# Performance work log

Hardware: AMD Instinct MI355X
Metric: run time of the kernel (lower is better)

## Reference

```python
import jax, jax.numpy as jnp
import numpy as np

H = 8        # num attention heads
DH = 160     # head dim (hidden_size // H)
HS = 1280    # hidden_size
CAD = 768    # cross_attention_dim
R = 4        # LoRA rank
LORA_SCALE = 1.0  # `scale` forward arg (default 1.0)


def setup_inputs() -> dict:
    key = jax.random.key(0)
    ks = jax.random.split(key, 16)
    rn = lambda k, s, std=0.02: (jax.random.normal(k, s) * std).astype(jnp.float32)
    return {
        "hidden_states": jax.random.normal(ks[0], (8, 4096, HS), jnp.float32),
        "encoder_hidden_states": jax.random.normal(ks[1], (8, 77, CAD), jnp.float32),
        # base attention projections (nn.Linear weight layout: [out, in])
        "Wq": rn(ks[2], (HS, HS)),
        "Wk": rn(ks[3], (HS, CAD)),
        "Wv": rn(ks[4], (HS, CAD)),
        "Wo": rn(ks[5], (HS, HS)),
        "bo": jnp.zeros((HS,), jnp.float32),
        # LoRA down/up pairs (down std ~ 1/rank; up nonzero so grads flow)
        "q_down": rn(ks[6], (R, HS), 0.25), "q_up": rn(ks[7], (HS, R)),
        "k_down": rn(ks[8], (R, CAD), 0.25), "k_up": rn(ks[9], (HS, R)),
        "v_down": rn(ks[10], (R, CAD), 0.25), "v_up": rn(ks[11], (HS, R)),
        "o_down": rn(ks[12], (R, HS), 0.25), "o_up": rn(ks[13], (HS, R)),
    }


def reference(hidden_states, encoder_hidden_states, Wq, Wk, Wv, Wo, bo,
              q_down, q_up, k_down, k_up, v_down, v_up, o_down, o_up):
    B, S, _ = hidden_states.shape
    T = encoder_hidden_states.shape[1]
    lora = lambda x, d, u: (x @ d.T) @ u.T  # LoRALinearLayer: up(down(x))

    q = hidden_states @ Wq.T + LORA_SCALE * lora(hidden_states, q_down, q_up)
    k = encoder_hidden_states @ Wk.T + LORA_SCALE * lora(encoder_hidden_states, k_down, k_up)
    v = encoder_hidden_states @ Wv.T + LORA_SCALE * lora(encoder_hidden_states, v_down, v_up)

    q = q.reshape(B, S, H, DH)
    k = k.reshape(B, T, H, DH)
    v = v.reshape(B, T, H, DH)

    # attn.get_attention_scores: scaled QK^T, softmax (no mask)
    inv_sqrt_d = jnp.asarray(1.0 / np.sqrt(DH), q.dtype)
    scores = jnp.einsum('bshd,bthd->bhst', q, k) * inv_sqrt_d
    probs = jax.nn.softmax(scores, axis=-1)
    o = jnp.einsum('bhst,bthd->bshd', probs, v).reshape(B, S, H * DH)

    # to_out[0] (Linear with bias) + LoRA on the same input; to_out[1] dropout = identity (eval)
    return o @ Wo.T + bo + LORA_SCALE * lora(o, o_down, o_up)
```

## Files before the change

kernel.cpp:

```cpp
#include <hip/hip_runtime.h>
#include <hip/hip_bf16.h>
#include <stdint.h>

typedef short bf16x8 __attribute__((ext_vector_type(8)));
typedef float f32x4 __attribute__((ext_vector_type(4)));

#define DEVI static __device__ __forceinline__

DEVI ushort f2bf(float f) {
  union { float f; uint32_t u; } v; v.f = f;
  uint32_t u = v.u;
  return (ushort)((u + 0x7fffu + ((u >> 16) & 1u)) >> 16);
}

DEVI void gload16(const void* g, void* l) {
  __builtin_amdgcn_global_load_lds((const __attribute__((address_space(1))) void*)g,
                                   (__attribute__((address_space(3))) void*)l,
                                   16, 0, 0);
}

#define SB() __builtin_amdgcn_sched_barrier(0)
#define BAR() __builtin_amdgcn_s_barrier()
#define MFMA(a, b, c) __builtin_amdgcn_mfma_f32_16x16x32_bf16((a), (b), (c), 0, 0, 0)
#define KEY4(r) ((((r) & 3)) ^ (((r) >> 2) & 3))

__global__ __launch_bounds__(256) void cvt_hs(const float* __restrict__ in,
                                              ushort* __restrict__ out) {
  const long step = 2048L * 256;
  for (long idx = (long)blockIdx.x * 256 + threadIdx.x; idx < 5242880; idx += step) {
    const float4* p = (const float4*)(in + idx * 8);
    float4 a = p[0], b = p[1];
    union { ushort us[8]; uint4 v; } r;
    r.us[0] = f2bf(a.x); r.us[1] = f2bf(a.y); r.us[2] = f2bf(a.z); r.us[3] = f2bf(a.w);
    r.us[4] = f2bf(b.x); r.us[5] = f2bf(b.y); r.us[6] = f2bf(b.z); r.us[7] = f2bf(b.w);
    *(uint4*)(out + idx * 8) = r.v;
  }
}

__global__ __launch_bounds__(256) void fold_t(
    const float* __restrict__ W, const float* __restrict__ up,
    const float* __restrict__ down, ushort* __restrict__ outT, float scale)
{
  __shared__ ushort tile[64][66];
  const int o0 = blockIdx.x * 64, i0 = blockIdx.y * 64;
  const int lo = threadIdx.x >> 6;
  const int li = threadIdx.x & 63;
#pragma unroll
  for (int r = 0; r < 16; ++r) {
    int o = o0 + r * 4 + lo;
    int i = i0 + li;
    float v = W[(long)o * 1280 + i];
#pragma unroll
    for (int q = 0; q < 4; ++q) v += up[o * 4 + q] * down[q * 1280 + i];
    tile[li][r * 4 + lo] = f2bf(v * scale);
  }
  __syncthreads();
#pragma unroll
  for (int r = 0; r < 16; ++r) {
    int i = i0 + r * 4 + lo;
    outT[(long)i * 1280 + o0 + li] = tile[r * 4 + lo][li];
  }
}

__global__ __launch_bounds__(256) void smalls(
    const float* __restrict__ ehs, ushort* __restrict__ ehs_bf,
    const float* __restrict__ Wk, const float* __restrict__ k_up, const float* __restrict__ k_down,
    const float* __restrict__ Wv, const float* __restrict__ v_up, const float* __restrict__ v_down,
    ushort* __restrict__ Wkv,
    const float* __restrict__ Wo, const float* __restrict__ o_up, const float* __restrict__ o_down,
    ushort* __restrict__ Wo_bf, ushort* __restrict__ Nt)
{
  const int b = blockIdx.x;
  const int tid = threadIdx.x;
  if (b < 231) {
    int idx = b * 256 + tid;
    if (idx < 59136) {
      const float4* p = (const float4*)(ehs + (long)idx * 8);
      float4 a = p[0], c = p[1];
      union { ushort us[8]; uint4 v; } r;
      r.us[0] = f2bf(a.x); r.us[1] = f2bf(a.y); r.us[2] = f2bf(a.z); r.us[3] = f2bf(a.w);
      r.us[4] = f2bf(c.x); r.us[5] = f2bf(c.y); r.us[6] = f2bf(c.z); r.us[7] = f2bf(c.w);
      *(uint4*)(ehs_bf + (long)idx * 8) = r.v;
    }
  } else if (b < 4071) {
    int idx = (b - 231) * 256 + tid;
    int o = idx / 768, i = idx - o * 768;
    float v = Wk[idx];
#pragma unroll
    for (int q = 0; q < 4; ++q) v += k_up[o * 4 + q] * k_down[q * 768 + i];
    Wkv[idx] = f2bf(v);
  } else if (b < 7911) {
    int idx = (b - 4071) * 256 + tid;
    int o = idx / 768, i = idx - o * 768;
    float v = Wv[idx];
#pragma unroll
    for (int q = 0; q < 4; ++q) v += v_up[o * 4 + q] * v_down[q * 768 + i];
    Wkv[983040 + idx] = f2bf(v);
  } else if (b < 14311) {
    int idx = (b - 7911) * 256 + tid;
    int o = idx / 1280, i = idx - o * 1280;
    float v = Wo[idx];
#pragma unroll
    for (int q = 0; q < 4; ++q) v += o_up[o * 4 + q] * o_down[q * 1280 + i];
    Wo_bf[idx] = f2bf(v);
  } else {
    int idx = (b - 14311) * 256 + tid;
    int bb = idx / (1280 * 24);
    int rem = idx % (1280 * 24);
    int j = rem / 24, q = rem % 24;
    int h = q / 3, t = 77 + q % 3;
    Nt[(long)bb * 1280 * 640 + (long)j * 640 + h * 80 + t] = 0;
  }
}


__global__ __launch_bounds__(256) void gemm_bt(
    const ushort* __restrict__ A, long sA0, long sA1, int lda, int validM,
    const ushort* __restrict__ B, long sB0, long sB1, int ldb, int validN,
    float* __restrict__ C32, ushort* __restrict__ C16, long sC0, long sC1, int ldc,
    const float* __restrict__ bias, int K)
{
  __shared__ ushort As[128 * 32];
  __shared__ ushort Bs[128 * 32];

  const int z = blockIdx.z;
  const ushort* Ab = A + (long)(z >> 3) * sA0 + (long)(z & 7) * sA1;
  const ushort* Bb = B + (long)(z >> 3) * sB0 + (long)(z & 7) * sB1;
  const int m0 = blockIdx.x * 128;
  const int n0 = blockIdx.y * 128;
  const int tid = threadIdx.x;
  const int lane = tid & 63;
  const int wid = tid >> 6;

  const int c0 = tid;
  const int arow0 = min(m0 + (c0 >> 2), validM - 1);
  const int arow1 = min(m0 + (c0 >> 2) + 64, validM - 1);
  const int brow0 = min(n0 + (c0 >> 2), validN - 1);
  const int brow1 = min(n0 + (c0 >> 2) + 64, validN - 1);
  const int seg = (c0 & 3) * 8;

  const int wr = (wid >> 1) * 64;
  const int wc = (wid & 1) * 64;
  const int frow = lane & 15;
  const int fk = (lane >> 4) * 8;

  f32x4 acc[4][4] = {};

  for (int kt = 0; kt < K; kt += 32) {
    gload16(Ab + (long)arow0 * lda + kt + seg, As + c0 * 8);
    gload16(Ab + (long)arow1 * lda + kt + seg, As + (c0 + 256) * 8);
    gload16(Bb + (long)brow0 * ldb + kt + seg, Bs + c0 * 8);
    gload16(Bb + (long)brow1 * ldb + kt + seg, Bs + (c0 + 256) * 8);
    __syncthreads();

    bf16x8 af[4], bfr[4];
#pragma unroll
    for (int m = 0; m < 4; ++m)
      af[m] = *(const bf16x8*)(As + (wr + m * 16 + frow) * 32 + fk);
#pragma unroll
    for (int n = 0; n < 4; ++n)
      bfr[n] = *(const bf16x8*)(Bs + (wc + n * 16 + frow) * 32 + fk);
#pragma unroll
    for (int m = 0; m < 4; ++m)
#pragma unroll
      for (int n = 0; n < 4; ++n)
        acc[m][n] = MFMA(af[m], bfr[n], acc[m][n]);
    __syncthreads();
  }

  const long cb = (long)(z >> 3) * sC0 + (long)(z & 7) * sC1;
  const int crow = m0 + wr + (lane >> 4) * 4;
  const int ccol = n0 + wc + (lane & 15);
#pragma unroll
  for (int m = 0; m < 4; ++m)
#pragma unroll
    for (int n = 0; n < 4; ++n)
#pragma unroll
      for (int j = 0; j < 4; ++j) {
        int r = crow + m * 16 + j;
        int c = ccol + n * 16;
        if (r < validM && c < validN) {
          float v = acc[m][n][j];
          if (bias) v += bias[c];
          if (C32) C32[cb + (long)r * ldc + c] = v;
          else     C16[cb + (long)r * ldc + c] = f2bf(v);
        }
      }
}

__global__ __launch_bounds__(256, 3) void score_softmax(
    const ushort* __restrict__ hsb, const ushort* __restrict__ Mt,
    ushort* __restrict__ probs)
{
  __shared__ ushort lds[22528];

  const int z = blockIdx.z;
  const int s0 = blockIdx.x * 128;
  const int h0 = blockIdx.y * 2;
  const int tid = threadIdx.x;
  const int lane = tid & 63;
  const int wid = tid >> 6;
  const int wM = wid >> 1;
  const int wN = wid & 1;
  const int l15 = lane & 15;
  const int l4 = lane >> 4;
  const int sl = tid & 3;

  const ushort* Ag = hsb + ((long)z * 4096 + s0) * 1280;
  long asrc[2]; int adst[2];
#pragma unroll
  for (int j = 0; j < 2; ++j) {
    int r = j * 64 + (tid >> 2);
    asrc[j] = (long)r * 1280 + ((sl ^ KEY4(r)) * 8);
    adst[j] = (j * 256 + tid) * 8;
  }
  const ushort* Bg = Mt + (long)z * (640L * 1280);
  long bsrc[3]; int bdst[3];
#pragma unroll
  for (int j = 0; j < 3; ++j) {
    int rb = j * 64 + (tid >> 2);
    int c = h0 * 96 + rb;
    int hh = c / 96, tt = min(c - hh * 96, 76);
    bsrc[j] = (long)(hh * 77 + tt) * 1280 + ((sl ^ KEY4(rb)) * 8);
    bdst[j] = 4096 + (j * 256 + tid) * 8;
  }

  int aoff[4], boff[6];
#pragma unroll
  for (int m = 0; m < 4; ++m) {
    int r = wM * 64 + m * 16 + l15;
    aoff[m] = r * 32 + ((l4 ^ KEY4(r)) * 8);
  }
#pragma unroll
  for (int n = 0; n < 6; ++n) {
    int r = wN * 96 + n * 16 + l15;
    boff[n] = 4096 + r * 32 + ((l4 ^ KEY4(r)) * 8);
  }

  f32x4 acc[4][6] = {};

#define SS_STAGE(bb, kt) { \
    _Pragma("unroll") for (int j = 0; j < 2; ++j) gload16(Ag + asrc[j] + (kt), &lds[(bb) + adst[j]]); \
    _Pragma("unroll") for (int j = 0; j < 3; ++j) gload16(Bg + bsrc[j] + (kt), &lds[(bb) + bdst[j]]); }

  SS_STAGE(0, 0)

  for (int t = 0; t < 40; ++t) {
    const int base = (t & 1) * 10240;
    if (t + 1 < 40) {
      SS_STAGE(10240 - base, (t + 1) * 32)
      asm volatile("s_waitcnt vmcnt(5)" ::: "memory");
    } else {
      asm volatile("s_waitcnt vmcnt(0)" ::: "memory");
    }
    SB(); BAR(); SB();
    bf16x8 av[4], bv[6];
#pragma unroll
    for (int m = 0; m < 4; ++m) av[m] = *(const bf16x8*)(&lds[base + aoff[m]]);
#pragma unroll
    for (int n = 0; n < 6; ++n) bv[n] = *(const bf16x8*)(&lds[base + boff[n]]);
    __builtin_amdgcn_s_setprio(1);
#pragma unroll
    for (int m = 0; m < 4; ++m)
#pragma unroll
      for (int n = 0; n < 6; ++n)
        acc[m][n] = MFMA(av[m], bv[n], acc[m][n]);
    __builtin_amdgcn_s_setprio(0);
    SB(); BAR();
  }
#undef SS_STAGE

#pragma unroll
  for (int m = 0; m < 4; ++m)
#pragma unroll
    for (int j = 0; j < 4; ++j) {
      float mx = -1e30f;
#pragma unroll
      for (int n = 0; n < 6; ++n)
        if (n * 16 + l15 < 77) mx = fmaxf(mx, acc[m][n][j]);
#pragma unroll
      for (int o = 8; o; o >>= 1) mx = fmaxf(mx, __shfl_xor(mx, o));
      float sum = 0.f;
#pragma unroll
      for (int n = 0; n < 6; ++n) {
        float e = (n * 16 + l15 < 77) ? __expf(acc[m][n][j] - mx) : 0.f;
        acc[m][n][j] = e;
        sum += e;
      }
#pragma unroll
      for (int o = 8; o; o >>= 1) sum += __shfl_xor(sum, o);
      float inv = 1.f / sum;
#pragma unroll
      for (int n = 0; n < 6; ++n) acc[m][n][j] *= inv;
    }

  __syncthreads();
  ushort* pw = lds + wid * 5632;
#pragma unroll
  for (int m = 0; m < 4; ++m)
#pragma unroll
    for (int n = 0; n < 5; ++n)
#pragma unroll
      for (int j = 0; j < 4; ++j)
        pw[(m * 16 + l4 * 4 + j) * 88 + n * 16 + l15] = f2bf(acc[m][n][j]);

  const uint* pw32 = (const uint*)pw;
  uint* probs32 = (uint*)probs;
  const int head = h0 + wN;
  const long sbase = (long)z * 4096 + s0 + wM * 64;
#pragma unroll 4
  for (int k = 0; k < 40; ++k) {
    int f2 = k * 64 + lane;
    int r = f2 / 40;
    int tp = f2 - r * 40;
    probs32[(sbase + r) * 320 + head * 40 + tp] = pw32[r * 44 + tp];
  }
}

__global__ __launch_bounds__(256, 4) void gemm_out(
    const ushort* __restrict__ P, const ushort* __restrict__ Nt,
    float* __restrict__ C, const float* __restrict__ bias)
{
  __shared__ ushort lds[16384];

  const int z = blockIdx.z;
  const ushort* Ab = P + (long)z * (4096L * 640) + (long)blockIdx.x * 128 * 640;
  const ushort* Bb = Nt + (long)z * (1280L * 640) + (long)blockIdx.y * 128 * 640;
  const int tid = threadIdx.x;
  const int lane = tid & 63;
  const int wid = tid >> 6;
  const int wM = wid >> 1;
  const int wN = wid & 1;
  const int l15 = lane & 15;
  const int l4 = lane >> 4;
  const int sl = tid & 3;

  long asrc[2]; int adst[2], bdst[2];
#pragma unroll
  for (int j = 0; j < 2; ++j) {
    int r = j * 64 + (tid >> 2);
    asrc[j] = (long)r * 640 + ((sl ^ KEY4(r)) * 8);
    adst[j] = (j * 256 + tid) * 8;
    bdst[j] = 4096 + (j * 256 + tid) * 8;
  }

  int aoff[4], boff[4];
#pragma unroll
  for (int m = 0; m < 4; ++m) {
    int r = wM * 64 + m * 16 + l15;
    aoff[m] = r * 32 + ((l4 ^ KEY4(r)) * 8);
  }
#pragma unroll
  for (int n = 0; n < 4; ++n) {
    int r = wN * 64 + n * 16 + l15;
    boff[n] = 4096 + r * 32 + ((l4 ^ KEY4(r)) * 8);
  }

  f32x4 acc[4][4] = {};

#define OG_STAGE(bb, kt) { \
    _Pragma("unroll") for (int j = 0; j < 2; ++j) gload16(Ab + asrc[j] + (kt), &lds[(bb) + adst[j]]); \
    _Pragma("unroll") for (int j = 0; j < 2; ++j) gload16(Bb + asrc[j] + (kt), &lds[(bb) + bdst[j]]); }

  OG_STAGE(0, 0)

  for (int t = 0; t < 20; ++t) {
    const int base = (t & 1) * 8192;
    if (t + 1 < 20) {
      OG_STAGE(8192 - base, (t + 1) * 32)
      asm volatile("s_waitcnt vmcnt(4)" ::: "memory");
    } else {
      asm volatile("s_waitcnt vmcnt(0)" ::: "memory");
    }
    SB(); BAR(); SB();
    bf16x8 av[4], bv[4];
#pragma unroll
    for (int m = 0; m < 4; ++m) av[m] = *(const bf16x8*)(&lds[base + aoff[m]]);
#pragma unroll
    for (int n = 0; n < 4; ++n) bv[n] = *(const bf16x8*)(&lds[base + boff[n]]);
    __builtin_amdgcn_s_setprio(1);
#pragma unroll
    for (int m = 0; m < 4; ++m)
#pragma unroll
      for (int n = 0; n < 4; ++n)
        acc[m][n] = MFMA(av[m], bv[n], acc[m][n]);
    __builtin_amdgcn_s_setprio(0);
    SB(); BAR();
  }
#undef OG_STAGE

  __syncthreads();
  float* pw = (float*)lds + wid * 1088;
  const int ccol = blockIdx.y * 128 + wN * 64;
  const float4 bv4 = *(const float4*)(bias + ccol + l15 * 4);
  const long crow0 = (long)z * 4096 + blockIdx.x * 128 + wM * 64;
#pragma unroll
  for (int m = 0; m < 4; ++m) {
#pragma unroll
    for (int n = 0; n < 4; ++n)
#pragma unroll
      for (int j = 0; j < 4; ++j)
        pw[(l4 * 4 + j) * 68 + n * 16 + l15] = acc[m][n][j];
    asm volatile("s_waitcnt lgkmcnt(0)" ::: "memory"); SB();
#pragma unroll
    for (int pass = 0; pass < 4; ++pass) {
      int r = pass * 4 + l4;
      float4 v = *(const float4*)(pw + r * 68 + l15 * 4);
      v.x += bv4.x; v.y += bv4.y; v.z += bv4.z; v.w += bv4.w;
      *(float4*)(C + (crow0 + m * 16 + r) * 1280 + ccol + l15 * 4) = v;
    }
    asm volatile("s_waitcnt lgkmcnt(0)" ::: "memory"); SB();
  }
}

extern "C" void kernel_launch(void* const* d_in, const int* in_sizes, int n_in,
                              void* d_out, int out_size, void* d_ws, size_t ws_size,
                              hipStream_t stream) {
  (void)in_sizes; (void)n_in; (void)out_size; (void)ws_size;
  const float* hs     = (const float*)d_in[0];
  const float* ehs    = (const float*)d_in[1];
  const float* Wq     = (const float*)d_in[2];
  const float* Wk     = (const float*)d_in[3];
  const float* Wv     = (const float*)d_in[4];
  const float* Wo     = (const float*)d_in[5];
  const float* bo     = (const float*)d_in[6];
  const float* q_down = (const float*)d_in[7];
  const float* q_up   = (const float*)d_in[8];
  const float* k_down = (const float*)d_in[9];
  const float* k_up   = (const float*)d_in[10];
  const float* v_down = (const float*)d_in[11];
  const float* v_up   = (const float*)d_in[12];
  const float* o_down = (const float*)d_in[13];
  const float* o_up   = (const float*)d_in[14];

  char* w = (char*)d_ws;
  size_t off = 0;
  auto alloc = [&](size_t b) { char* p = w + off; off = (off + b + 255) & ~(size_t)255; return p; };
  ushort* hs_bf  = (ushort*)alloc(32768L * 1280 * 2);
  ushort* ehs_bf = (ushort*)alloc(616L * 768 * 2);
  ushort* WqT    = (ushort*)alloc(1280L * 1280 * 2);
  ushort* Wkv    = (ushort*)alloc(2560L * 768 * 2);
  ushort* Wo_bf  = (ushort*)alloc(1280L * 1280 * 2);
  ushort* kv_bf  = (ushort*)alloc(616L * 2560 * 2);
  ushort* Mt     = (ushort*)alloc(8L * 640 * 1280 * 2);
  ushort* Nt     = (ushort*)alloc(8L * 1280 * 640 * 2);
  ushort* probs  = (ushort*)alloc(8L * 4096 * 640 * 2);
  float*  outp   = (float*)d_out;
  const float invs = 0.07905694150420949f;

  cvt_hs<<<2048, 256, 0, stream>>>(hs, hs_bf);
  fold_t<<<dim3(20, 20), 256, 0, stream>>>(Wq, q_up, q_down, WqT, invs);
  smalls<<<15271, 256, 0, stream>>>(ehs, ehs_bf,
      Wk, k_up, k_down, Wv, v_up, v_down, Wkv,
      Wo, o_up, o_down, Wo_bf, Nt);
  gemm_bt<<<dim3(5, 20, 1), 256, 0, stream>>>(ehs_bf, 0, 0, 768, 616,
      Wkv, 0, 0, 768, 2560, nullptr, kv_bf, 0, 0, 2560, nullptr, 768);
  gemm_bt<<<dim3(1, 10, 64), 256, 0, stream>>>(kv_bf, 77L * 2560, 160, 2560, 77,
      WqT, 0, 160, 1280, 1280, nullptr, Mt, 640L * 1280, 77L * 1280, 1280, nullptr, 160);
  gemm_bt<<<dim3(10, 1, 64), 256, 0, stream>>>(Wo_bf, 0, 160, 1280, 1280,
      kv_bf + 1280, 77L * 2560, 160, 2560, 77, nullptr, Nt, 1280L * 640, 80, 640, nullptr, 160);
  score_softmax<<<dim3(32, 4, 8), 256, 0, stream>>>(hs_bf, Mt, probs);
  gemm_out<<<dim3(32, 10, 8), 256, 0, stream>>>(probs, Nt, outp, bo);
}
```

Baseline: 283.7 us.

## Merge prep kernels and Mt/Nt GEMMs, switch LDS swizzle to paired-row layout

Folds the hs conversion, Wq fold/transpose and small-weight prep into one prep launch, and runs the two per-head Mt and Nt GEMMs in a single launch. This removes several kernel launches and their tail gaps. It also replaces the KEY4 XOR swizzle in score_softmax and gemm_out with a two-rows-per-64-element paired layout meant to reduce LDS bank conflicts. gemm_out gets a larger LDS array, which may lower occupancy.

```diff
diff --git a/kernel.cpp b/kernel.cpp
--- a/kernel.cpp
+++ b/kernel.cpp
@@ -22,47 +22,22 @@
 #define SB() __builtin_amdgcn_sched_barrier(0)
 #define BAR() __builtin_amdgcn_s_barrier()
 #define MFMA(a, b, c) __builtin_amdgcn_mfma_f32_16x16x32_bf16((a), (b), (c), 0, 0, 0)
-#define KEY4(r) ((((r) & 3)) ^ (((r) >> 2) & 3))
-
-__global__ __launch_bounds__(256) void cvt_hs(const float* __restrict__ in,
-                                              ushort* __restrict__ out) {
-  const long step = 2048L * 256;
-  for (long idx = (long)blockIdx.x * 256 + threadIdx.x; idx < 5242880; idx += step) {
-    const float4* p = (const float4*)(in + idx * 8);
-    float4 a = p[0], b = p[1];
-    union { ushort us[8]; uint4 v; } r;
-    r.us[0] = f2bf(a.x); r.us[1] = f2bf(a.y); r.us[2] = f2bf(a.z); r.us[3] = f2bf(a.w);
-    r.us[4] = f2bf(b.x); r.us[5] = f2bf(b.y); r.us[6] = f2bf(b.z); r.us[7] = f2bf(b.w);
-    *(uint4*)(out + idx * 8) = r.v;
-  }
-}
-
-__global__ __launch_bounds__(256) void fold_t(
-    const float* __restrict__ W, const float* __restrict__ up,
-    const float* __restrict__ down, ushort* __restrict__ outT, float scale)
-{
-  __shared__ ushort tile[64][66];
-  const int o0 = blockIdx.x * 64, i0 = blockIdx.y * 64;
-  const int lo = threadIdx.x >> 6;
-  const int li = threadIdx.x & 63;
-#pragma unroll
-  for (int r = 0; r < 16; ++r) {
-    int o = o0 + r * 4 + lo;
-    int i = i0 + li;
-    float v = W[(long)o * 1280 + i];
-#pragma unroll
-    for (int q = 0; q < 4; ++q) v += up[o * 4 + q] * down[q * 1280 + i];
-    tile[li][r * 4 + lo] = f2bf(v * scale);
-  }
-  __syncthreads();
-#pragma unroll
-  for (int r = 0; r < 16; ++r) {
-    int i = i0 + r * 4 + lo;
-    outT[(long)i * 1280 + o0 + li] = tile[r * 4 + lo][li];
-  }
-}
-
-__global__ __launch_bounds__(256) void smalls(
+
+DEVI int pair_src_row(int c, int* k8) {
+  int pair = c >> 3;
+  int s = (c & 7) ^ (pair & 7);
+  *k8 = s >> 1;
+  return pair * 2 + (s & 1);
+}
+DEVI int pair_frag_off(int r, int k8) {
+  int p = (k8 * 2 + (r & 1)) ^ ((r >> 1) & 7);
+  return (r >> 1) * 64 + p * 8;
+}
+
+__global__ __launch_bounds__(256) void prep(
+    const float* __restrict__ hs, ushort* __restrict__ hs_bf,
+    const float* __restrict__ Wq, const float* __restrict__ q_up, const float* __restrict__ q_down,
+    ushort* __restrict__ WqT, float scale,
     const float* __restrict__ ehs, ushort* __restrict__ ehs_bf,
     const float* __restrict__ Wk, const float* __restrict__ k_up, const float* __restrict__ k_down,
     const float* __restrict__ Wv, const float* __restrict__ v_up, const float* __restrict__ v_down,
@@ -70,64 +45,94 @@
     const float* __restrict__ Wo, const float* __restrict__ o_up, const float* __restrict__ o_down,
     ushort* __restrict__ Wo_bf, ushort* __restrict__ Nt)
 {
+  __shared__ ushort tile[64][66];
   const int b = blockIdx.x;
   const int tid = threadIdx.x;
-  if (b < 231) {
-    int idx = b * 256 + tid;
-    if (idx < 59136) {
-      const float4* p = (const float4*)(ehs + (long)idx * 8);
+  if (b < 2048) {
+    const long step = 2048L * 256;
+    for (long idx = (long)b * 256 + tid; idx < 5242880; idx += step) {
+      const float4* p = (const float4*)(hs + idx * 8);
       float4 a = p[0], c = p[1];
       union { ushort us[8]; uint4 v; } r;
       r.us[0] = f2bf(a.x); r.us[1] = f2bf(a.y); r.us[2] = f2bf(a.z); r.us[3] = f2bf(a.w);
       r.us[4] = f2bf(c.x); r.us[5] = f2bf(c.y); r.us[6] = f2bf(c.z); r.us[7] = f2bf(c.w);
-      *(uint4*)(ehs_bf + (long)idx * 8) = r.v;
-    }
-  } else if (b < 4071) {
-    int idx = (b - 231) * 256 + tid;
-    int o = idx / 768, i = idx - o * 768;
-    float v = Wk[idx];
-#pragma unroll
-    for (int q = 0; q < 4; ++q) v += k_up[o * 4 + q] * k_down[q * 768 + i];
-    Wkv[idx] = f2bf(v);
-  } else if (b < 7911) {
-    int idx = (b - 4071) * 256 + tid;
-    int o = idx / 768, i = idx - o * 768;
-    float v = Wv[idx];
-#pragma unroll
-    for (int q = 0; q < 4; ++q) v += v_up[o * 4 + q] * v_down[q * 768 + i];
-    Wkv[983040 + idx] = f2bf(v);
-  } else if (b < 14311) {
-    int idx = (b - 7911) * 256 + tid;
-    int o = idx / 1280, i = idx - o * 1280;
-    float v = Wo[idx];
-#pragma unroll
-    for (int q = 0; q < 4; ++q) v += o_up[o * 4 + q] * o_down[q * 1280 + i];
-    Wo_bf[idx] = f2bf(v);
+      *(uint4*)(hs_bf + idx * 8) = r.v;
+    }
+  } else if (b < 2448) {
+    const int fb = b - 2048;
+    const int o0 = (fb / 20) * 64, i0 = (fb % 20) * 64;
+    const int lo = tid >> 6;
+    const int li = tid & 63;
+#pragma unroll
+    for (int r = 0; r < 16; ++r) {
+      int o = o0 + r * 4 + lo;
+      int i = i0 + li;
+      float v = Wq[(long)o * 1280 + i];
+#pragma unroll
+      for (int q = 0; q < 4; ++q) v += q_up[o * 4 + q] * q_down[q * 1280 + i];
+      tile[li][r * 4 + lo] = f2bf(v * scale);
+    }
+    __syncthreads();
+#pragma unroll
+    for (int r = 0; r < 16; ++r) {
+      int i = i0 + r * 4 + lo;
+      WqT[(long)i * 1280 + o0 + li] = tile[r * 4 + lo][li];
+    }
   } else {
-    int idx = (b - 14311) * 256 + tid;
-    int bb = idx / (1280 * 24);
-    int rem = idx % (1280 * 24);
-    int j = rem / 24, q = rem % 24;
-    int h = q / 3, t = 77 + q % 3;
-    Nt[(long)bb * 1280 * 640 + (long)j * 640 + h * 80 + t] = 0;
-  }
-}
-
-
-__global__ __launch_bounds__(256) void gemm_bt(
+    const int sb = b - 2448;
+    if (sb < 231) {
+      int idx = sb * 256 + tid;
+      if (idx < 59136) {
+        const float4* p = (const float4*)(ehs + (long)idx * 8);
+        float4 a = p[0], c = p[1];
+        union { ushort us[8]; uint4 v; } r;
+        r.us[0] = f2bf(a.x); r.us[1] = f2bf(a.y); r.us[2] = f2bf(a.z); r.us[3] = f2bf(a.w);
+        r.us[4] = f2bf(c.x); r.us[5] = f2bf(c.y); r.us[6] = f2bf(c.z); r.us[7] = f2bf(c.w);
+        *(uint4*)(ehs_bf + (long)idx * 8) = r.v;
+      }
+    } else if (sb < 4071) {
+      int idx = (sb - 231) * 256 + tid;
+      int o = idx / 768, i = idx - o * 768;
+      float v = Wk[idx];
+#pragma unroll
+      for (int q = 0; q < 4; ++q) v += k_up[o * 4 + q] * k_down[q * 768 + i];
+      Wkv[idx] = f2bf(v);
+    } else if (sb < 7911) {
+      int idx = (sb - 4071) * 256 + tid;
+      int o = idx / 768, i = idx - o * 768;
+      float v = Wv[idx];
+#pragma unroll
+      for (int q = 0; q < 4; ++q) v += v_up[o * 4 + q] * v_down[q * 768 + i];
+      Wkv[983040 + idx] = f2bf(v);
+    } else if (sb < 14311) {
+      int idx = (sb - 7911) * 256 + tid;
+      int o = idx / 1280, i = idx - o * 1280;
+      float v = Wo[idx];
+#pragma unroll
+      for (int q = 0; q < 4; ++q) v += o_up[o * 4 + q] * o_down[q * 1280 + i];
+      Wo_bf[idx] = f2bf(v);
+    } else {
+      int idx = (sb - 14311) * 256 + tid;
+      int bb = idx / (1280 * 24);
+      int rem = idx % (1280 * 24);
+      int j = rem / 24, q = rem % 24;
+      int h = q / 3, t = 77 + q % 3;
+      Nt[(long)bb * 1280 * 640 + (long)j * 640 + h * 80 + t] = 0;
+    }
+  }
+}
+
+
+DEVI void gemm_bt_body(int bx, int by, int z,
     const ushort* __restrict__ A, long sA0, long sA1, int lda, int validM,
     const ushort* __restrict__ B, long sB0, long sB1, int ldb, int validN,
     float* __restrict__ C32, ushort* __restrict__ C16, long sC0, long sC1, int ldc,
-    const float* __restrict__ bias, int K)
-{
-  __shared__ ushort As[128 * 32];
-  __shared__ ushort Bs[128 * 32];
-
-  const int z = blockIdx.z;
+    const float* __restrict__ bias, int K, ushort* As, ushort* Bs)
+{
   const ushort* Ab = A + (long)(z >> 3) * sA0 + (long)(z & 7) * sA1;
   const ushort* Bb = B + (long)(z >> 3) * sB0 + (long)(z & 7) * sB1;
-  const int m0 = blockIdx.x * 128;
-  const int n0 = blockIdx.y * 128;
+  const int m0 = bx * 128;
+  const int n0 = by * 128;
   const int tid = threadIdx.x;
   const int lane = tid & 63;
   const int wid = tid >> 6;
@@ -188,6 +193,37 @@
       }
 }
 
+__global__ __launch_bounds__(256) void gemm_bt(
+    const ushort* A, long sA0, long sA1, int lda, int validM,
+    const ushort* B, long sB0, long sB1, int ldb, int validN,
+    float* C32, ushort* C16, long sC0, long sC1, int ldc,
+    const float* bias, int K)
+{
+  __shared__ ushort As[128 * 32];
+  __shared__ ushort Bs[128 * 32];
+  gemm_bt_body(blockIdx.x, blockIdx.y, blockIdx.z,
+               A, sA0, sA1, lda, validM, B, sB0, sB1, ldb, validN,
+               C32, C16, sC0, sC1, ldc, bias, K, As, Bs);
+}
+
+__global__ __launch_bounds__(256) void gemm_mtnt(
+    const ushort* __restrict__ kv_bf, const ushort* __restrict__ WqT,
+    const ushort* __restrict__ Wo_bf, ushort* __restrict__ Mt, ushort* __restrict__ Nt)
+{
+  __shared__ ushort As[128 * 32];
+  __shared__ ushort Bs[128 * 32];
+  const int x = blockIdx.x, z = blockIdx.z;
+  if (x < 10) {
+    gemm_bt_body(x, 0, z, Wo_bf, 0, 160, 1280, 1280,
+                 kv_bf + 1280, 77L * 2560, 160, 2560, 77,
+                 nullptr, Nt, 1280L * 640, 80, 640, nullptr, 160, As, Bs);
+  } else {
+    gemm_bt_body(0, x - 10, z, kv_bf, 77L * 2560, 160, 2560, 77,
+                 WqT, 0, 160, 1280, 1280,
+                 nullptr, Mt, 640L * 1280, 77L * 1280, 1280, nullptr, 160, As, Bs);
+  }
+}
+
 __global__ __launch_bounds__(256, 3) void score_softmax(
     const ushort* __restrict__ hsb, const ushort* __restrict__ Mt,
     ushort* __restrict__ probs)
@@ -204,38 +240,35 @@
   const int wN = wid & 1;
   const int l15 = lane & 15;
   const int l4 = lane >> 4;
-  const int sl = tid & 3;
 
   const ushort* Ag = hsb + ((long)z * 4096 + s0) * 1280;
   long asrc[2]; int adst[2];
 #pragma unroll
   for (int j = 0; j < 2; ++j) {
-    int r = j * 64 + (tid >> 2);
-    asrc[j] = (long)r * 1280 + ((sl ^ KEY4(r)) * 8);
-    adst[j] = (j * 256 + tid) * 8;
+    int c = j * 256 + tid, k8;
+    int r = pair_src_row(c, &k8);
+    asrc[j] = (long)r * 1280 + k8 * 8;
+    adst[j] = c * 8;
   }
   const ushort* Bg = Mt + (long)z * (640L * 1280);
   long bsrc[3]; int bdst[3];
 #pragma unroll
   for (int j = 0; j < 3; ++j) {
-    int rb = j * 64 + (tid >> 2);
-    int c = h0 * 96 + rb;
-    int hh = c / 96, tt = min(c - hh * 96, 76);
-    bsrc[j] = (long)(hh * 77 + tt) * 1280 + ((sl ^ KEY4(rb)) * 8);
-    bdst[j] = 4096 + (j * 256 + tid) * 8;
+    int c = j * 256 + tid, k8;
+    int rb = pair_src_row(c, &k8);
+    int hh = h0 + (rb >= 96);
+    int tt = min(rb - 96 * (rb >= 96), 76);
+    bsrc[j] = (long)(hh * 77 + tt) * 1280 + k8 * 8;
+    bdst[j] = 4096 + c * 8;
   }
 
   int aoff[4], boff[6];
 #pragma unroll
-  for (int m = 0; m < 4; ++m) {
-    int r = wM * 64 + m * 16 + l15;
-    aoff[m] = r * 32 + ((l4 ^ KEY4(r)) * 8);
-  }
-#pragma unroll
-  for (int n = 0; n < 6; ++n) {
-    int r = wN * 96 + n * 16 + l15;
-    boff[n] = 4096 + r * 32 + ((l4 ^ KEY4(r)) * 8);
-  }
+  for (int m = 0; m < 4; ++m)
+    aoff[m] = pair_frag_off(wM * 64 + m * 16 + l15, l4);
+#pragma unroll
+  for (int n = 0; n < 6; ++n)
+    boff[n] = 4096 + pair_frag_off(wN * 96 + n * 16 + l15, l4);
 
   f32x4 acc[4][6] = {};
 
@@ -321,7 +354,7 @@
     const ushort* __restrict__ P, const ushort* __restrict__ Nt,
     float* __restrict__ C, const float* __restrict__ bias)
 {
-  __shared__ ushort lds[16384];
+  __shared__ ushort lds[17408];
 
   const int z = blockIdx.z;
   const ushort* Ab = P + (long)z * (4096L * 640) + (long)blockIdx.x * 128 * 640;
@@ -333,28 +366,24 @@
   const int wN = wid & 1;
   const int l15 = lane & 15;
   const int l4 = lane >> 4;
-  const int sl = tid & 3;
 
   long asrc[2]; int adst[2], bdst[2];
 #pragma unroll
   for (int j = 0; j < 2; ++j) {
-    int r = j * 64 + (tid >> 2);
-    asrc[j] = (long)r * 640 + ((sl ^ KEY4(r)) * 8);
-    adst[j] = (j * 256 + tid) * 8;
-    bdst[j] = 4096 + (j * 256 + tid) * 8;
+    int c = j * 256 + tid, k8;
+    int r = pair_src_row(c, &k8);
+    asrc[j] = (long)r * 640 + k8 * 8;
+    adst[j] = c * 8;
+    bdst[j] = 4096 + c * 8;
   }
 
   int aoff[4], boff[4];
 #pragma unroll
-  for (int m = 0; m < 4; ++m) {
-    int r = wM * 64 + m * 16 + l15;
-    aoff[m] = r * 32 + ((l4 ^ KEY4(r)) * 8);
-  }
-#pragma unroll
-  for (int n = 0; n < 4; ++n) {
-    int r = wN * 64 + n * 16 + l15;
-    boff[n] = 4096 + r * 32 + ((l4 ^ KEY4(r)) * 8);
-  }
+  for (int m = 0; m < 4; ++m)
+    aoff[m] = pair_frag_off(wM * 64 + m * 16 + l15, l4);
+#pragma unroll
+  for (int n = 0; n < 4; ++n)
+    boff[n] = 4096 + pair_frag_off(wN * 64 + n * 16 + l15, l4);
 
   f32x4 acc[4][4] = {};
 
@@ -448,17 +477,12 @@
   float*  outp   = (float*)d_out;
   const float invs = 0.07905694150420949f;
 
-  cvt_hs<<<2048, 256, 0, stream>>>(hs, hs_bf);
-  fold_t<<<dim3(20, 20), 256, 0, stream>>>(Wq, q_up, q_down, WqT, invs);
-  smalls<<<15271, 256, 0, stream>>>(ehs, ehs_bf,
-      Wk, k_up, k_down, Wv, v_up, v_down, Wkv,
+  prep<<<17719, 256, 0, stream>>>(hs, hs_bf, Wq, q_up, q_down, WqT, invs,
+      ehs, ehs_bf, Wk, k_up, k_down, Wv, v_up, v_down, Wkv,
       Wo, o_up, o_down, Wo_bf, Nt);
   gemm_bt<<<dim3(5, 20, 1), 256, 0, stream>>>(ehs_bf, 0, 0, 768, 616,
       Wkv, 0, 0, 768, 2560, nullptr, kv_bf, 0, 0, 2560, nullptr, 768);
-  gemm_bt<<<dim3(1, 10, 64), 256, 0, stream>>>(kv_bf, 77L * 2560, 160, 2560, 77,
-      WqT, 0, 160, 1280, 1280, nullptr, Mt, 640L * 1280, 77L * 1280, 1280, nullptr, 160);
-  gemm_bt<<<dim3(10, 1, 64), 256, 0, stream>>>(Wo_bf, 0, 160, 1280, 1280,
-      kv_bf + 1280, 77L * 2560, 160, 2560, 77, nullptr, Nt, 1280L * 640, 80, 640, nullptr, 160);
+  gemm_mtnt<<<dim3(20, 1, 64), 256, 0, stream>>>(kv_bf, WqT, Wo_bf, Mt, Nt);
   score_softmax<<<dim3(32, 4, 8), 256, 0, stream>>>(hs_bf, Mt, probs);
   gemm_out<<<dim3(32, 10, 8), 256, 0, stream>>>(probs, Nt, outp, bo);
 }
```

Result: slower. 297.3 us (+4.8%).
